# Kernel optimization log

Measured on AMD Instinct MI355X. Metric: run time of the kernel, lower is better.

Reference implementation:

```python
import jax, jax.numpy as jnp
import numpy as np

B, S, H, K = 64, 512, 768, 64
NR, NN, ND = 9, 3, 3


def setup_inputs() -> dict:
    key = jax.random.key(0)
    ks = jax.random.split(key, 20)
    inp = {}
    inp["sequence_output"] = jax.random.normal(ks[0], (B, S, H), jnp.float32)
    for i, name in enumerate(["rel", "nov", "dir"]):
        inp[f"{name}_idx"] = jax.random.randint(ks[1 + i], (B, K), 0, S)
        inp[f"{name}_len"] = jax.random.randint(ks[4 + i], (B,), 0, K + 1)
    scale = 0.02
    for i, (name, nlab) in enumerate([("rel", NR), ("nov", NN), ("dir", ND)]):
        k0, k1 = jax.random.split(ks[7 + i])
        inp[f"{name}_dense_W"] = scale * jax.random.normal(k0, (H, H), jnp.float32)
        inp[f"{name}_dense_b"] = jnp.zeros((H,), jnp.float32)
        inp[f"{name}_cls_W"] = scale * jax.random.normal(k1, (nlab, H), jnp.float32)
        inp[f"{name}_cls_b"] = jnp.zeros((nlab,), jnp.float32)
    return inp


def _attn_pool(seq, idx, length):
    """Ragged intra-group self-attention pooling (get_token_reps / get_ne_reps).

    seq: [B,S,H]; idx: [B,K] padded token indices; length: [B] valid counts.
    Original computes (softmax(G G^T) @ G)[0]; only row 0 of the attention is
    needed, so we compute just that row.
    """
    G = jnp.take_along_axis(seq, idx[:, :, None], axis=1)  # [B,K,H]
    mask = jnp.arange(idx.shape[1])[None, :] < length[:, None]  # [B,K]
    scores0 = jnp.einsum('bh,bjh->bj', G[:, 0], G)  # row 0 of G G^T
    scores0 = jnp.where(mask, scores0, jnp.float32(-1e30))
    a0 = jax.nn.softmax(scores0, axis=-1)  # [B,K]
    pooled = jnp.einsum('bj,bjh->bh', a0, G)  # [B,H]
    # empty-group fallback: sequence_output[b, 0]
    return jnp.where(length[:, None] > 0, pooled, seq[:, 0])


def _head(rep, Wd, bd, Wc, bc):
    # HiddenTokenPooler dense + tanh, then token classifier
    h = jnp.tanh(rep @ Wd.T + bd)
    return h @ Wc.T + bc


def reference(sequence_output, rel_idx, rel_len, nov_idx, nov_len, dir_idx, dir_len,
              rel_dense_W, rel_dense_b, rel_cls_W, rel_cls_b,
              nov_dense_W, nov_dense_b, nov_cls_W, nov_cls_b,
              dir_dense_W, dir_dense_b, dir_cls_W, dir_cls_b):
    rel_rep = _attn_pool(sequence_output, rel_idx, rel_len)
    nov_rep = _attn_pool(sequence_output, nov_idx, nov_len)
    dir_rep = _attn_pool(sequence_output, dir_idx, dir_len)
    rel_logits = _head(rel_rep, rel_dense_W, rel_dense_b, rel_cls_W, rel_cls_b)
    nov_logits = _head(nov_rep, nov_dense_W, nov_dense_b, nov_cls_W, nov_cls_b)
    dir_logits = _head(dir_rep, dir_dense_W, dir_dense_b, dir_cls_W, dir_cls_b)
    return (rel_logits, nov_logits, dir_logits)
```

## Files before the change

### kernel.cpp

```cpp
#include <hip/hip_runtime.h>
#include <math.h>


#define Hdim 768
#define Kdim 64
#define Sdim 512
#define Bdim 64
#define LDK  72

typedef float f32x4 __attribute__((ext_vector_type(4)));
typedef short bf16x8 __attribute__((ext_vector_type(8)));

__device__ __forceinline__ unsigned short f2bf(float f) {
    union { float f; unsigned int u; } c; c.f = f;
    unsigned int u = c.u + 0x7FFFu + ((c.u >> 16) & 1u);
    return (unsigned short)(u >> 16);
}

__global__ __launch_bounds__(1024) void k_pool(
    const float* __restrict__ seq,
    const int* __restrict__ idxr, const int* __restrict__ lenr,
    const int* __restrict__ idxn, const int* __restrict__ lenn,
    const int* __restrict__ idxd, const int* __restrict__ lend,
    const float* __restrict__ cbr, const float* __restrict__ cbn,
    const float* __restrict__ cbd,
    float* __restrict__ pooled,
    float* __restrict__ out)
{
    const int b = blockIdx.x, g = blockIdx.y;
    const int tid = threadIdx.x, lane = tid & 63, wave = tid >> 6;

    const int* idxp = (g == 0) ? idxr : (g == 1) ? idxn : idxd;
    const int* lnp  = (g == 0) ? lenr : (g == 1) ? lenn : lend;

    __shared__ int   sidx[Kdim];
    __shared__ float wm[16], wl[16], coef[16];
    __shared__ float wpart[16][Hdim];

    if (tid < Kdim) sidx[tid] = idxp[b * Kdim + tid];
    const int len = lnp[b];

    if (b == 0) {
        if (g == 0)      { if (tid < 576) out[tid]       = cbr[tid % 9]; }
        else if (g == 1) { if (tid < 192) out[576 + tid] = cbn[tid % 3]; }
        else             { if (tid < 192) out[768 + tid] = cbd[tid % 3]; }
    }
    __syncthreads();

    float* dst = pooled + ((size_t)g * Bdim + b) * Hdim;

    if (len > 0) {
        const float* row0 = seq + ((size_t)b * Sdim + sidx[0]) * Hdim;
        float g0[12];
#pragma unroll
        for (int k = 0; k < 3; ++k) {
            float4 t = *(const float4*)(row0 + 4 * lane + 256 * k);
            g0[4 * k + 0] = t.x; g0[4 * k + 1] = t.y;
            g0[4 * k + 2] = t.z; g0[4 * k + 3] = t.w;
        }

        float v[4][12];
#pragma unroll
        for (int t = 0; t < 4; ++t)
#pragma unroll
            for (int k = 0; k < 12; ++k) v[t][k] = 0.f;

#pragma unroll
        for (int t = 0; t < 4; ++t) {
            int j = wave + 16 * t;
            if (j < len) {
                const float* rowj = seq + ((size_t)b * Sdim + sidx[j]) * Hdim + 4 * lane;
#pragma unroll
                for (int k = 0; k < 3; ++k) {
                    float4 x = *(const float4*)(rowj + 256 * k);
                    v[t][4 * k + 0] = x.x; v[t][4 * k + 1] = x.y;
                    v[t][4 * k + 2] = x.z; v[t][4 * k + 3] = x.w;
                }
            }
        }

        float s[4];
#pragma unroll
        for (int t = 0; t < 4; ++t) {
            float a = 0.f;
#pragma unroll
            for (int k = 0; k < 12; ++k) a += g0[k] * v[t][k];
            s[t] = a;
        }
#pragma unroll
        for (int off = 32; off > 0; off >>= 1)
#pragma unroll
            for (int t = 0; t < 4; ++t) s[t] += __shfl_xor(s[t], off, 64);

#pragma unroll
        for (int t = 0; t < 4; ++t)
            if (wave + 16 * t >= len) s[t] = -1e30f;

        float m = fmaxf(fmaxf(s[0], s[1]), fmaxf(s[2], s[3]));
        float e[4], l = 0.f;
#pragma unroll
        for (int t = 0; t < 4; ++t) {
            e[t] = (wave + 16 * t < len) ? __expf(s[t] - m) : 0.f;
            l += e[t];
        }
        float p[12];
#pragma unroll
        for (int k = 0; k < 12; ++k)
            p[k] = e[0] * v[0][k] + e[1] * v[1][k] + e[2] * v[2][k] + e[3] * v[3][k];

        if (lane == 0) { wm[wave] = m; wl[wave] = l; }
#pragma unroll
        for (int k = 0; k < 3; ++k)
            *(float4*)&wpart[wave][4 * lane + 256 * k] =
                make_float4(p[4 * k], p[4 * k + 1], p[4 * k + 2], p[4 * k + 3]);
        __syncthreads();

        if (wave == 0 && lane < 16) {
            float mw = wm[lane], lw = wl[lane];
            float M = mw;
#pragma unroll
            for (int off = 8; off > 0; off >>= 1) M = fmaxf(M, __shfl_xor(M, off, 64));
            float sc = __expf(mw - M);
            float Ls = lw * sc;
#pragma unroll
            for (int off = 8; off > 0; off >>= 1) Ls += __shfl_xor(Ls, off, 64);
            coef[lane] = sc / Ls;
        }
        __syncthreads();

        if (tid < Hdim) {
            float acc = 0.f;
#pragma unroll
            for (int w = 0; w < 16; ++w) acc += wpart[w][tid] * coef[w];
            dst[tid] = acc;
        }
    } else {
        if (tid < Hdim) dst[tid] = seq[(size_t)b * Sdim * Hdim + tid];
    }
}

__global__ __launch_bounds__(256) void k_dense_cls(
    const float* __restrict__ pooled,
    const float* __restrict__ dWr, const float* __restrict__ dbr,
    const float* __restrict__ cWr,
    const float* __restrict__ dWn, const float* __restrict__ dbn,
    const float* __restrict__ cWn,
    const float* __restrict__ dWd, const float* __restrict__ dbd,
    const float* __restrict__ cWd,
    float* __restrict__ out)
{
    const int mt = blockIdx.x, g = blockIdx.y;
    const float *dW, *db, *cW; int nlab, off;
    if (g == 0)      { dW = dWr; db = dbr; cW = cWr; nlab = 9; off = 0;   }
    else if (g == 1) { dW = dWn; db = dbn; cW = cWn; nlab = 3; off = 576; }
    else             { dW = dWd; db = dbd; cW = cWd; nlab = 3; off = 768; }
    const int i0 = mt * 64;

    const int tid = threadIdx.x, lane = tid & 63, wv = tid >> 6;
    const int q = lane >> 4, col = lane & 15;

    __shared__ unsigned short Ws[64 * LDK];
    __shared__ unsigned short Ps[64 * LDK];
    __shared__ float hs[64][65];

    f32x4 acc[4] = {{0,0,0,0},{0,0,0,0},{0,0,0,0},{0,0,0,0}};

    const int srow  = tid >> 2;
    const int cbase = (tid & 3) * 16;
    const float* Pg = pooled + (size_t)g * Bdim * Hdim;

    for (int kk = 0; kk < Hdim; kk += 64) {
#pragma unroll
        for (int u = 0; u < 4; ++u) {
            int c = cbase + 4 * u;
            float4 w4 = *(const float4*)(dW + (size_t)(i0 + srow) * Hdim + kk + c);
            float4 p4 = *(const float4*)(Pg + (size_t)srow * Hdim + kk + c);
            *(ushort4*)&Ws[srow * LDK + c] = make_ushort4(f2bf(w4.x), f2bf(w4.y), f2bf(w4.z), f2bf(w4.w));
            *(ushort4*)&Ps[srow * LDK + c] = make_ushort4(f2bf(p4.x), f2bf(p4.y), f2bf(p4.z), f2bf(p4.w));
        }
        __syncthreads();
#pragma unroll
        for (int ks = 0; ks < 64; ks += 32) {
            bf16x8 a = *(const bf16x8*)&Ws[(wv * 16 + col) * LDK + ks + 8 * q];
#pragma unroll
            for (int n = 0; n < 4; ++n) {
                bf16x8 bb = *(const bf16x8*)&Ps[(n * 16 + col) * LDK + ks + 8 * q];
                acc[n] = __builtin_amdgcn_mfma_f32_16x16x32_bf16(a, bb, acc[n], 0, 0, 0);
            }
        }
        __syncthreads();
    }

#pragma unroll
    for (int n = 0; n < 4; ++n) {
        int bb = n * 16 + col;
#pragma unroll
        for (int r = 0; r < 4; ++r) {
            int il = wv * 16 + q * 4 + r;
            hs[il][bb] = tanhf(acc[n][r] + db[i0 + il]);
        }
    }
    __syncthreads();

    for (int c = wv; c < nlab; c += 4) {
        const float* wr = cW + (size_t)c * Hdim + i0;
        float a = 0.f;
#pragma unroll 16
        for (int il = 0; il < 64; ++il)
            a += wr[il] * hs[il][lane];
        atomicAdd(&out[off + lane * nlab + c], a);
    }
}

extern "C" void kernel_launch(void* const* d_in, const int* in_sizes, int n_in,
                              void* d_out, int out_size, void* d_ws, size_t ws_size,
                              hipStream_t stream) {
    const float* seq  = (const float*)d_in[0];
    const int*   idxr = (const int*)d_in[1];
    const int*   lenr = (const int*)d_in[2];
    const int*   idxn = (const int*)d_in[3];
    const int*   lenn = (const int*)d_in[4];
    const int*   idxd = (const int*)d_in[5];
    const int*   lend = (const int*)d_in[6];
    const float* dWr  = (const float*)d_in[7];
    const float* dbr  = (const float*)d_in[8];
    const float* cWr  = (const float*)d_in[9];
    const float* cbr  = (const float*)d_in[10];
    const float* dWn  = (const float*)d_in[11];
    const float* dbn  = (const float*)d_in[12];
    const float* cWn  = (const float*)d_in[13];
    const float* cbn  = (const float*)d_in[14];
    const float* dWd  = (const float*)d_in[15];
    const float* dbd  = (const float*)d_in[16];
    const float* cWd  = (const float*)d_in[17];
    const float* cbd  = (const float*)d_in[18];
    float* out = (float*)d_out;

    float* pooled = (float*)d_ws;

    k_pool<<<dim3(Bdim, 3), 1024, 0, stream>>>(
        seq, idxr, lenr, idxn, lenn, idxd, lend, cbr, cbn, cbd, pooled, out);
    k_dense_cls<<<dim3(Hdim / 64, 3), 256, 0, stream>>>(
        pooled, dWr, dbr, cWr, dWn, dbn, cWn, dWd, dbd, cWd, out);
}
```

Baseline: 190.7 us.

## Pre-convert dense weights and pooled reps to bf16, split-K dense GEMM

The pool kernel now also converts the three dense weight matrices to bf16 in workspace and writes the pooled representations as bf16. The dense kernel loads its A tiles straight into registers and the full pooled B matrix into swizzled LDS, dropping the per-K-step sync loop. It uses 512 threads with a two-way K split reduced through shared memory. This trades extra conversion work in the pool kernel, which is memory bound, for less conversion and fewer barriers in the GEMM. It also adds roughly 110KB of LDS per block.

```diff
diff --git a/kernel.cpp b/kernel.cpp
--- a/kernel.cpp
+++ b/kernel.cpp
@@ -6,7 +6,6 @@
 #define Kdim 64
 #define Sdim 512
 #define Bdim 64
-#define LDK  72
 
 typedef float f32x4 __attribute__((ext_vector_type(4)));
 typedef short bf16x8 __attribute__((ext_vector_type(8)));
@@ -22,9 +21,12 @@
     const int* __restrict__ idxr, const int* __restrict__ lenr,
     const int* __restrict__ idxn, const int* __restrict__ lenn,
     const int* __restrict__ idxd, const int* __restrict__ lend,
+    const float* __restrict__ dWr, const float* __restrict__ dWn,
+    const float* __restrict__ dWd,
     const float* __restrict__ cbr, const float* __restrict__ cbn,
     const float* __restrict__ cbd,
-    float* __restrict__ pooled,
+    unsigned short* __restrict__ dWb,
+    unsigned short* __restrict__ pooledb,
     float* __restrict__ out)
 {
     const int b = blockIdx.x, g = blockIdx.y;
@@ -47,7 +49,7 @@
     }
     __syncthreads();
 
-    float* dst = pooled + ((size_t)g * Bdim + b) * Hdim;
+    unsigned short* pb = pooledb + ((size_t)g * Bdim + b) * Hdim;
 
     if (len > 0) {
         const float* row0 = seq + ((size_t)b * Sdim + sidx[0]) * Hdim;
@@ -132,77 +134,102 @@
             float acc = 0.f;
 #pragma unroll
             for (int w = 0; w < 16; ++w) acc += wpart[w][tid] * coef[w];
-            dst[tid] = acc;
+            pb[tid] = f2bf(acc);
         }
     } else {
-        if (tid < Hdim) dst[tid] = seq[(size_t)b * Sdim * Hdim + tid];
-    }
-}
-
-__global__ __launch_bounds__(256) void k_dense_cls(
-    const float* __restrict__ pooled,
-    const float* __restrict__ dWr, const float* __restrict__ dbr,
-    const float* __restrict__ cWr,
-    const float* __restrict__ dWn, const float* __restrict__ dbn,
-    const float* __restrict__ cWn,
-    const float* __restrict__ dWd, const float* __restrict__ dbd,
-    const float* __restrict__ cWd,
+        if (tid < Hdim) pb[tid] = f2bf(seq[(size_t)b * Sdim * Hdim + tid]);
+    }
+
+    {
+        const float* dWsrc = (g == 0) ? dWr : (g == 1) ? dWn : dWd;
+        unsigned short* dWdst = dWb + (size_t)g * Hdim * Hdim;
+        if (tid < Hdim) {
+#pragma unroll
+            for (int r = 0; r < 12; ++r) {
+                size_t o = (size_t)(b * 12 + r) * Hdim + tid;
+                dWdst[o] = f2bf(dWsrc[o]);
+            }
+        }
+    }
+}
+
+__global__ __launch_bounds__(512) void k_dense_cls(
+    const unsigned short* __restrict__ dWb,
+    const unsigned short* __restrict__ pooledb,
+    const float* __restrict__ dbr, const float* __restrict__ cWr,
+    const float* __restrict__ dbn, const float* __restrict__ cWn,
+    const float* __restrict__ dbd, const float* __restrict__ cWd,
     float* __restrict__ out)
 {
     const int mt = blockIdx.x, g = blockIdx.y;
-    const float *dW, *db, *cW; int nlab, off;
-    if (g == 0)      { dW = dWr; db = dbr; cW = cWr; nlab = 9; off = 0;   }
-    else if (g == 1) { dW = dWn; db = dbn; cW = cWn; nlab = 3; off = 576; }
-    else             { dW = dWd; db = dbd; cW = cWd; nlab = 3; off = 768; }
+    const float *db, *cW; int nlab, off;
+    if (g == 0)      { db = dbr; cW = cWr; nlab = 9; off = 0;   }
+    else if (g == 1) { db = dbn; cW = cWn; nlab = 3; off = 576; }
+    else             { db = dbd; cW = cWd; nlab = 3; off = 768; }
     const int i0 = mt * 64;
 
     const int tid = threadIdx.x, lane = tid & 63, wv = tid >> 6;
-    const int q = lane >> 4, col = lane & 15;
-
-    __shared__ unsigned short Ws[64 * LDK];
-    __shared__ unsigned short Ps[64 * LDK];
+    const int col = lane & 15, q = lane >> 4;
+    const int kq = wv >> 2, m = wv & 3;
+
+    __shared__ __align__(16) char PsB[64 * 1536];
+    __shared__ float P1[64][65];
     __shared__ float hs[64][65];
 
+    const unsigned short* Ag = dWb + (size_t)g * Hdim * Hdim;
+    const unsigned short* ab = Ag + (size_t)(i0 + m * 16 + col) * Hdim + kq * 384 + q * 8;
+    bf16x8 a_reg[12];
+#pragma unroll
+    for (int ks = 0; ks < 12; ++ks)
+        a_reg[ks] = *(const bf16x8*)(ab + ks * 32);
+
+    {
+        const unsigned short* Pg = pooledb + (size_t)g * Bdim * Hdim;
+        const int row = tid >> 3, seg = tid & 7;
+        const unsigned short* src = Pg + (size_t)row * Hdim + seg * 8;
+        const int rb = row * 1536, sw = (row & 7) << 4;
+#pragma unroll
+        for (int j = 0; j < 12; ++j) {
+            bf16x8 v = *(const bf16x8*)(src + j * 64);
+            *(bf16x8*)(PsB + ((rb + j * 128 + seg * 16) ^ sw)) = v;
+        }
+    }
+    __syncthreads();
+
     f32x4 acc[4] = {{0,0,0,0},{0,0,0,0},{0,0,0,0},{0,0,0,0}};
-
-    const int srow  = tid >> 2;
-    const int cbase = (tid & 3) * 16;
-    const float* Pg = pooled + (size_t)g * Bdim * Hdim;
-
-    for (int kk = 0; kk < Hdim; kk += 64) {
-#pragma unroll
-        for (int u = 0; u < 4; ++u) {
-            int c = cbase + 4 * u;
-            float4 w4 = *(const float4*)(dW + (size_t)(i0 + srow) * Hdim + kk + c);
-            float4 p4 = *(const float4*)(Pg + (size_t)srow * Hdim + kk + c);
-            *(ushort4*)&Ws[srow * LDK + c] = make_ushort4(f2bf(w4.x), f2bf(w4.y), f2bf(w4.z), f2bf(w4.w));
-            *(ushort4*)&Ps[srow * LDK + c] = make_ushort4(f2bf(p4.x), f2bf(p4.y), f2bf(p4.z), f2bf(p4.w));
-        }
-        __syncthreads();
-#pragma unroll
-        for (int ks = 0; ks < 64; ks += 32) {
-            bf16x8 a = *(const bf16x8*)&Ws[(wv * 16 + col) * LDK + ks + 8 * q];
-#pragma unroll
-            for (int n = 0; n < 4; ++n) {
-                bf16x8 bb = *(const bf16x8*)&Ps[(n * 16 + col) * LDK + ks + 8 * q];
-                acc[n] = __builtin_amdgcn_mfma_f32_16x16x32_bf16(a, bb, acc[n], 0, 0, 0);
+#pragma unroll
+    for (int ks = 0; ks < 12; ++ks) {
+#pragma unroll
+        for (int n = 0; n < 4; ++n) {
+            const int row = n * 16 + col;
+            const int bo = (row * 1536 + kq * 768 + ks * 64 + q * 16) ^ ((row & 7) << 4);
+            bf16x8 bb = *(const bf16x8*)(PsB + bo);
+            acc[n] = __builtin_amdgcn_mfma_f32_16x16x32_bf16(a_reg[ks], bb, acc[n], 0, 0, 0);
+        }
+    }
+
+    if (kq == 1) {
+#pragma unroll
+        for (int n = 0; n < 4; ++n)
+#pragma unroll
+            for (int r = 0; r < 4; ++r)
+                P1[m * 16 + q * 4 + r][n * 16 + col] = acc[n][r];
+    }
+    __syncthreads();
+    if (kq == 0) {
+#pragma unroll
+        for (int n = 0; n < 4; ++n) {
+            const int bb2 = n * 16 + col;
+#pragma unroll
+            for (int r = 0; r < 4; ++r) {
+                const int il = m * 16 + q * 4 + r;
+                hs[il][bb2] = tanhf(acc[n][r] + P1[il][bb2] + db[i0 + il]);
             }
         }
-        __syncthreads();
-    }
-
-#pragma unroll
-    for (int n = 0; n < 4; ++n) {
-        int bb = n * 16 + col;
-#pragma unroll
-        for (int r = 0; r < 4; ++r) {
-            int il = wv * 16 + q * 4 + r;
-            hs[il][bb] = tanhf(acc[n][r] + db[i0 + il]);
-        }
-    }
-    __syncthreads();
-
-    for (int c = wv; c < nlab; c += 4) {
+    }
+    __syncthreads();
+
+    for (int c = wv; c < nlab; c += 8) {
         const float* wr = cW + (size_t)c * Hdim + i0;
         float a = 0.f;
 #pragma unroll 16
@@ -236,10 +263,12 @@
     const float* cbd  = (const float*)d_in[18];
     float* out = (float*)d_out;
 
-    float* pooled = (float*)d_ws;
+    unsigned short* dWb     = (unsigned short*)d_ws;
+    unsigned short* pooledb = (unsigned short*)((char*)d_ws + (size_t)3 * Hdim * Hdim * 2);
 
     k_pool<<<dim3(Bdim, 3), 1024, 0, stream>>>(
-        seq, idxr, lenr, idxn, lenn, idxd, lend, cbr, cbn, cbd, pooled, out);
-    k_dense_cls<<<dim3(Hdim / 64, 3), 256, 0, stream>>>(
-        pooled, dWr, dbr, cWr, dWn, dbn, cWn, dWd, dbd, cWd, out);
-}
+        seq, idxr, lenr, idxn, lenn, idxd, lend,
+        dWr, dWn, dWd, cbr, cbn, cbd, dWb, pooledb, out);
+    k_dense_cls<<<dim3(Hdim / 64, 3), 512, 0, stream>>>(
+        dWb, pooledb, dbr, cWr, dbn, cWn, dbd, cWd, out);
+}
```

New measurement: 181.1 us, median of 2. 5.0% less time.
